# Kernel tuning notes

Hardware: AMD Instinct MI355X
Metric: run time of the kernel (lower is better)

The kernel has to match this reference:

```python
import jax, jax.numpy as jnp
import numpy as np

D_STATE = 16
D_CONV = 4
TOKEN = 8
GROUPS = 4
EPS = 1e-5


def _gn(x, w, b):
    # GroupNorm(GROUPS) over [B,C,H,W]
    B, C, H, W = x.shape
    xr = x.reshape(B, GROUPS, C // GROUPS, H * W)
    mu = xr.mean((2, 3), keepdims=True)
    var = xr.var((2, 3), keepdims=True)
    xn = ((xr - mu) * jax.lax.rsqrt(var + EPS)).reshape(B, C, H, W)
    return xn * w[None, :, None, None] + b[None, :, None, None]


def _mamba(x, in_w, conv_w, conv_b, xp_w, dt_w, dt_b, A_log, Dp, out_w, dt_rank):
    # mamba_ssm Mamba forward: x [B, L, d_model]
    Bn, L, _ = x.shape
    d_inner = conv_w.shape[0]
    xz = jnp.einsum('bld,ed->ble', x, in_w)          # [B,L,2*d_inner]
    xc, z = jnp.split(xz, 2, axis=-1)
    # causal depthwise conv1d (pad left d_conv-1)
    xt = jnp.pad(jnp.transpose(xc, (0, 2, 1)), ((0, 0), (0, 0), (D_CONV - 1, 0)))
    xt = jax.lax.conv_general_dilated(xt, conv_w[:, None, :], (1,), 'VALID',
                                      dimension_numbers=('NCH', 'OIH', 'NCH'),
                                      feature_group_count=d_inner)
    xc = jax.nn.silu(jnp.transpose(xt, (0, 2, 1)) + conv_b)
    dbl = jnp.einsum('ble,fe->blf', xc, xp_w)        # [B,L,dt_rank+2*d_state]
    dt = dbl[..., :dt_rank]
    Bm = dbl[..., dt_rank:dt_rank + D_STATE]
    Cm = dbl[..., dt_rank + D_STATE:]
    delta = jax.nn.softplus(jnp.einsum('blr,er->ble', dt, dt_w) + dt_b)
    A = -jnp.exp(A_log)                              # [d_inner, d_state]

    def step(h, inp):
        u_t, d_t, b_t, c_t = inp                     # [B,d_inner],[B,d_inner],[B,d_state],[B,d_state]
        dA = jnp.exp(d_t[..., None] * A)
        h = h * dA + (d_t * u_t)[..., None] * b_t[:, None, :]
        return h, jnp.sum(h * c_t[:, None, :], axis=-1)

    xs = (jnp.transpose(xc, (1, 0, 2)), jnp.transpose(delta, (1, 0, 2)),
          jnp.transpose(Bm, (1, 0, 2)), jnp.transpose(Cm, (1, 0, 2)))
    h0 = jnp.zeros((Bn, d_inner, D_STATE), x.dtype)
    _, ys = jax.lax.scan(step, h0, xs)
    y = (jnp.transpose(ys, (1, 0, 2)) + xc * Dp) * jax.nn.silu(z)
    return jnp.einsum('ble,de->bld', y, out_w)


def _mamba_params(key, d_model, dt_rank):
    d_inner = 2 * d_model
    ks = jax.random.split(key, 5)
    p = {}
    p['in_w'] = jax.random.normal(ks[0], (2 * d_inner, d_model)) / np.sqrt(d_model).astype(np.float32)
    p['conv_w'] = jax.random.normal(ks[1], (d_inner, D_CONV)) * 0.3
    p['conv_b'] = jnp.zeros((d_inner,))
    p['xp_w'] = jax.random.normal(ks[2], (dt_rank + 2 * D_STATE, d_inner)) / np.sqrt(d_inner).astype(np.float32)
    p['dt_w'] = jax.random.normal(ks[3], (d_inner, dt_rank)) / np.sqrt(dt_rank).astype(np.float32)
    p['dt_b'] = jnp.full((d_inner,), float(np.log(np.expm1(0.01))))
    p['A_log'] = jnp.log(jnp.broadcast_to(jnp.arange(1, D_STATE + 1, dtype=jnp.float32), (d_inner, D_STATE)))
    p['D'] = jnp.ones((d_inner,))
    p['out_w'] = jax.random.normal(ks[4], (d_model, d_inner)) / np.sqrt(d_inner).astype(np.float32)
    return p


def setup_inputs() -> dict:
    key = jax.random.key(0)
    k1, k2, k3 = jax.random.split(key, 3)
    B, C, H, W = 2, 64, 128, 128
    inp = {'x': jax.random.normal(k1, (B, C, H, W), dtype=jnp.float32)}
    spa = _mamba_params(k2, C, 4)
    spe = _mamba_params(k3, C // TOKEN, 1)
    for n, p in (('spa', spa), ('spe', spe)):
        for k, v in p.items():
            inp[f'{n}_{k}'] = v
    inp['spa_gn_w'] = jnp.ones((C,)); inp['spa_gn_b'] = jnp.zeros((C,))
    inp['spe_gn_w'] = jnp.ones((C,)); inp['spe_gn_b'] = jnp.zeros((C,))
    inp['fuse_w'] = jnp.full((2,), 0.5)
    return inp


def reference(x, spa_in_w, spa_conv_w, spa_conv_b, spa_xp_w, spa_dt_w, spa_dt_b,
              spa_A_log, spa_D, spa_out_w, spe_in_w, spe_conv_w, spe_conv_b,
              spe_xp_w, spe_dt_w, spe_dt_b, spe_A_log, spe_D, spe_out_w,
              spa_gn_w, spa_gn_b, spe_gn_w, spe_gn_b, fuse_w):
    B, C, H, W = x.shape
    # SpaMamba: scan over flattened spatial sequence
    xs = jnp.transpose(x, (0, 2, 3, 1)).reshape(B, H * W, C)
    ys = _mamba(xs, spa_in_w, spa_conv_w, spa_conv_b, spa_xp_w, spa_dt_w, spa_dt_b,
                spa_A_log, spa_D, spa_out_w, 4)
    spa = jnp.transpose(ys.reshape(B, H, W, C), (0, 3, 1, 2))
    spa = jax.nn.silu(_gn(spa, spa_gn_w, spa_gn_b)) + x
    # SpeMamba: scan over channel tokens per pixel (C == TOKEN * gc, no padding)
    gc = C // TOKEN
    xe = jnp.transpose(x, (0, 2, 3, 1)).reshape(B * H * W, TOKEN, gc)
    ye = _mamba(xe, spe_in_w, spe_conv_w, spe_conv_b, spe_xp_w, spe_dt_w, spe_dt_b,
                spe_A_log, spe_D, spe_out_w, 1)
    spe = jnp.transpose(ye.reshape(B, H, W, C), (0, 3, 1, 2))
    spe = jax.nn.silu(_gn(spe, spe_gn_w, spe_gn_b)) + x
    w = jax.nn.softmax(fuse_w)
    return spa * w[0] + spe * w[1] + x
```

## Files before the change

### kernel.cpp

```cpp
#include <hip/hip_runtime.h>
#include <math.h>


#define NB 2
#define NC 64
#define HW_ 16384
#define SCH 256
#define SLC 64

__device__ __forceinline__ float sigmoidf_(float v) { return 1.f / (1.f + __expf(-v)); }
__device__ __forceinline__ float siluf_(float v)    { return v * sigmoidf_(v); }
__device__ __forceinline__ float softplusf_(float v) {
    return v > 0.f ? v + log1pf(__expf(-v)) : log1pf(__expf(v));
}

#define K1_XS_OFF 8576
#define K1_XS_STR 68
#define K1_XCL_STR 132

__global__ __launch_bounds__(256) void k1_spatial_pre(
    const float* __restrict__ x, const float* __restrict__ in_w,
    const float* __restrict__ conv_w, const float* __restrict__ conv_b,
    const float* __restrict__ xp_w, const float* __restrict__ dt_w,
    const float* __restrict__ dt_b,
    float* __restrict__ xc_g, float* __restrict__ sz_g,
    float* __restrict__ delta_g, float* __restrict__ Bm_g, float* __restrict__ Cm_g)
{
    __shared__ float smem[13132];
    __shared__ float dtl[256];
    const int tid = threadIdx.x;
    const int b   = blockIdx.x >> 8;
    const int l0  = (blockIdx.x & 255) << 6;

    for (int i = tid; i < 67 * 64; i += 256) {
        int c = i / 67;
        int tok = i - c * 67;
        int l = l0 + tok - 3;
        float v = (l >= 0) ? x[((size_t)b * NC + c) * HW_ + l] : 0.f;
        smem[K1_XS_OFF + tok * K1_XS_STR + c] = v;
    }
    __syncthreads();

    {
        const int e = tid & 127;
        const int half = tid >> 7;
        float w[64];
        #pragma unroll
        for (int q = 0; q < 16; ++q) {
            float4 wv = *(const float4*)(in_w + e * 64 + q * 4);
            w[q*4] = wv.x; w[q*4+1] = wv.y; w[q*4+2] = wv.z; w[q*4+3] = wv.w;
        }
        int t0 = half ? 34 : 0, t1 = half ? 67 : 34;
        for (int tok = t0; tok < t1; ++tok) {
            const float4* xr = (const float4*)(smem + K1_XS_OFF + tok * K1_XS_STR);
            float acc = 0.f;
            #pragma unroll
            for (int q = 0; q < 16; ++q) {
                float4 xv = xr[q];
                acc += w[q*4]*xv.x + w[q*4+1]*xv.y + w[q*4+2]*xv.z + w[q*4+3]*xv.w;
            }
            smem[tok * 128 + e] = acc;
        }
        #pragma unroll
        for (int q = 0; q < 16; ++q) {
            float4 wv = *(const float4*)(in_w + (128 + e) * 64 + q * 4);
            w[q*4] = wv.x; w[q*4+1] = wv.y; w[q*4+2] = wv.z; w[q*4+3] = wv.w;
        }
        int z0 = half * 32;
        for (int tok = z0; tok < z0 + 32; ++tok) {
            const float4* xr = (const float4*)(smem + K1_XS_OFF + (tok + 3) * K1_XS_STR);
            float acc = 0.f;
            #pragma unroll
            for (int q = 0; q < 16; ++q) {
                float4 xv = xr[q];
                acc += w[q*4]*xv.x + w[q*4+1]*xv.y + w[q*4+2]*xv.z + w[q*4+3]*xv.w;
            }
            sz_g[((size_t)(b * HW_ + l0 + tok)) * 128 + e] = siluf_(acc);
        }
    }
    __syncthreads();

    {
        const int e = tid & 127;
        float cw0 = conv_w[e*4], cw1 = conv_w[e*4+1], cw2 = conv_w[e*4+2], cw3 = conv_w[e*4+3];
        float cb = conv_b[e];
        float r[32];
        #pragma unroll
        for (int k = 0; k < 32; ++k) {
            int tok = (tid + k * 256) >> 7;
            float v = cb + cw0 * smem[(tok+0)*128 + e] + cw1 * smem[(tok+1)*128 + e]
                         + cw2 * smem[(tok+2)*128 + e] + cw3 * smem[(tok+3)*128 + e];
            v = siluf_(v);
            r[k] = v;
            xc_g[((size_t)(b * HW_ + l0 + tok)) * 128 + e] = v;
        }
        __syncthreads();
        #pragma unroll
        for (int k = 0; k < 32; ++k) {
            int tok = (tid + k * 256) >> 7;
            smem[tok * K1_XCL_STR + e] = r[k];
        }
    }
    __syncthreads();

    for (int i = tid; i < 64 * 32; i += 256) {
        int tok = i >> 5;
        int f = i & 31;
        const float4* xr = (const float4*)(smem + tok * K1_XCL_STR);
        const float4* wr = (const float4*)(xp_w + (4 + f) * 128);
        float acc = 0.f;
        #pragma unroll
        for (int q = 0; q < 32; ++q) {
            float4 a = xr[q], w4 = wr[q];
            acc += a.x*w4.x + a.y*w4.y + a.z*w4.z + a.w*w4.w;
        }
        size_t row = (size_t)(b * HW_ + l0 + tok);
        if (f < 16) Bm_g[row * 16 + f] = acc;
        else        Cm_g[row * 16 + (f - 16)] = acc;
    }
    {
        int tok = tid >> 2;
        int rr = tid & 3;
        const float4* xr = (const float4*)(smem + tok * K1_XCL_STR);
        const float4* wr = (const float4*)(xp_w + rr * 128);
        float acc = 0.f;
        #pragma unroll
        for (int q = 0; q < 32; ++q) {
            float4 a = xr[q], w4 = wr[q];
            acc += a.x*w4.x + a.y*w4.y + a.z*w4.z + a.w*w4.w;
        }
        dtl[tid] = acc;
    }
    __syncthreads();
    {
        const int e = tid & 127;
        float w0 = dt_w[e*4], w1 = dt_w[e*4+1], w2 = dt_w[e*4+2], w3 = dt_w[e*4+3];
        float bb = dt_b[e];
        #pragma unroll
        for (int k = 0; k < 32; ++k) {
            int tok = (tid + k * 256) >> 7;
            float4 dv = *(const float4*)(dtl + tok * 4);
            float v = bb + w0*dv.x + w1*dv.y + w2*dv.z + w3*dv.w;
            delta_g[((size_t)(b * HW_ + l0 + tok)) * 128 + e] = softplusf_(v);
        }
    }
}

__global__ __launch_bounds__(256) void k2_scan1(
    const float* __restrict__ delta_g, const float* __restrict__ xc_g,
    const float* __restrict__ Bm_g, const float* __restrict__ A_log,
    float* __restrict__ cumA_g, float* __restrict__ hsum_g)
{
    const int tid = threadIdx.x;
    const int b = blockIdx.x >> 8;
    const int ch = blockIdx.x & 255;
    const int e = tid >> 1;
    const int n0 = (tid & 1) * 8;
    float A[8];
    #pragma unroll
    for (int j = 0; j < 8; ++j) A[j] = -__expf(A_log[e * 16 + n0 + j]);
    float h[8], cA[8];
    #pragma unroll
    for (int j = 0; j < 8; ++j) { h[j] = 0.f; cA[j] = 1.f; }
    const size_t rowbase = (size_t)b * HW_ + ch * SLC;
    for (int t = 0; t < SLC; ++t) {
        size_t row = rowbase + t;
        float d = delta_g[row * 128 + e];
        float u = xc_g[row * 128 + e];
        float4 b0 = *(const float4*)(Bm_g + row * 16 + n0);
        float4 b1 = *(const float4*)(Bm_g + row * 16 + n0 + 4);
        float Bv[8]; *(float4*)(Bv) = b0; *(float4*)(Bv + 4) = b1;
        float du = d * u;
        #pragma unroll
        for (int j = 0; j < 8; ++j) {
            float dA = __expf(d * A[j]);
            h[j] = h[j] * dA + du * Bv[j];
            cA[j] *= dA;
        }
    }
    size_t so = ((size_t)(b * SCH + ch)) * 2048 + tid * 8;
    #pragma unroll
    for (int j = 0; j < 8; ++j) { cumA_g[so + j] = cA[j]; hsum_g[so + j] = h[j]; }
}

__global__ __launch_bounds__(256) void k3_combine(
    const float* __restrict__ cumA_g, const float* __restrict__ hsum_g,
    float* __restrict__ Hin_g)
{
    int gid = blockIdx.x * 256 + threadIdx.x;
    int b = gid >> 11;
    int en = gid & 2047;
    float st = 0.f;
    size_t o = (size_t)b * SCH * 2048 + en;
    for (int cb = 0; cb < SCH; cb += 16) {
        float a[16], hs[16];
        #pragma unroll
        for (int k = 0; k < 16; ++k) {
            a[k]  = cumA_g[o + (size_t)k * 2048];
            hs[k] = hsum_g[o + (size_t)k * 2048];
        }
        #pragma unroll
        for (int k = 0; k < 16; ++k) {
            Hin_g[o + (size_t)k * 2048] = st;
            st = st * a[k] + hs[k];
        }
        o += (size_t)16 * 2048;
    }
}

__global__ __launch_bounds__(256) void k4_scan2(
    const float* __restrict__ delta_g, const float* __restrict__ xc_g,
    const float* __restrict__ sz_g, const float* __restrict__ Bm_g,
    const float* __restrict__ Cm_g, const float* __restrict__ A_log,
    const float* __restrict__ Dp, const float* __restrict__ Hin_g,
    const float* __restrict__ out_w,
    float* __restrict__ spa_raw, float* __restrict__ part_spa)
{
    __shared__ float ytile[SLC * 128];
    __shared__ float otile[64 * 65];
    __shared__ float wred[32];
    const int tid = threadIdx.x;
    const int b = blockIdx.x >> 8;
    const int ch = blockIdx.x & 255;
    const int e = tid >> 1;
    const int nh = tid & 1;
    const int n0 = nh * 8;
    float A[8];
    #pragma unroll
    for (int j = 0; j < 8; ++j) A[j] = -__expf(A_log[e * 16 + n0 + j]);
    float Dv = Dp[e];
    float h[8];
    size_t so = ((size_t)(b * SCH + ch)) * 2048 + tid * 8;
    #pragma unroll
    for (int j = 0; j < 8; ++j) h[j] = Hin_g[so + j];
    const size_t rowbase = (size_t)b * HW_ + ch * SLC;
    for (int t = 0; t < SLC; ++t) {
        size_t row = rowbase + t;
        float d = delta_g[row * 128 + e];
        float u = xc_g[row * 128 + e];
        float4 b0 = *(const float4*)(Bm_g + row * 16 + n0);
        float4 b1 = *(const float4*)(Bm_g + row * 16 + n0 + 4);
        float4 c0 = *(const float4*)(Cm_g + row * 16 + n0);
        float4 c1 = *(const float4*)(Cm_g + row * 16 + n0 + 4);
        float Bv[8]; *(float4*)(Bv) = b0; *(float4*)(Bv + 4) = b1;
        float Cv[8]; *(float4*)(Cv) = c0; *(float4*)(Cv + 4) = c1;
        float du = d * u;
        float y = 0.f;
        #pragma unroll
        for (int j = 0; j < 8; ++j) {
            float dA = __expf(d * A[j]);
            h[j] = h[j] * dA + du * Bv[j];
            y += h[j] * Cv[j];
        }
        y += __shfl_xor(y, 1, 64);
        if (nh == 0) {
            float szv = sz_g[row * 128 + e];
            ytile[t * 128 + e] = (y + u * Dv) * szv;
        }
    }
    __syncthreads();
    for (int i = tid; i < 64 * SLC; i += 256) {
        int c = i & 63, t = i >> 6;
        const float4* wr = (const float4*)(out_w + c * 128);
        const float4* yr = (const float4*)(ytile + t * 128);
        float acc = 0.f;
        #pragma unroll
        for (int q = 0; q < 32; ++q) {
            float4 w4 = wr[q], yv4 = yr[q];
            acc += w4.x*yv4.x + w4.y*yv4.y + w4.z*yv4.z + w4.w*yv4.w;
        }
        otile[c * 65 + t] = acc;
    }
    __syncthreads();
    for (int i = tid; i < 64 * SLC; i += 256) {
        int c = i >> 6, t = i & 63;
        spa_raw[((size_t)b * NC + c) * HW_ + ch * SLC + t] = otile[c * 65 + t];
    }
    float s[4], s2[4];
    #pragma unroll
    for (int g = 0; g < 4; ++g) {
        float a = 0.f, a2 = 0.f;
        for (int i = tid; i < 1024; i += 256) {
            int c = 16 * g + (i >> 6), t = i & 63;
            float v = otile[c * 65 + t];
            a += v; a2 += v * v;
        }
        s[g] = a; s2[g] = a2;
    }
    #pragma unroll
    for (int g = 0; g < 4; ++g) {
        #pragma unroll
        for (int o = 1; o < 64; o <<= 1) {
            s[g]  += __shfl_xor(s[g], o, 64);
            s2[g] += __shfl_xor(s2[g], o, 64);
        }
    }
    if ((tid & 63) == 0) {
        int w = tid >> 6;
        #pragma unroll
        for (int g = 0; g < 4; ++g) { wred[w*8 + g*2] = s[g]; wred[w*8 + g*2 + 1] = s2[g]; }
    }
    __syncthreads();
    if (tid < 8)
        part_spa[blockIdx.x * 8 + tid] = wred[tid] + wred[8+tid] + wred[16+tid] + wred[24+tid];
}

__global__ __launch_bounds__(256, 2) void k5_spectral(
    const float* __restrict__ x, const float* __restrict__ in_w,
    const float* __restrict__ conv_w, const float* __restrict__ conv_b,
    const float* __restrict__ xp_w, const float* __restrict__ dt_w,
    const float* __restrict__ dt_b, const float* __restrict__ A_log,
    const float* __restrict__ Dp, const float* __restrict__ out_w,
    float* __restrict__ spe_raw, float* __restrict__ part_spe)
{
    __shared__ float xin[16 * 65];
    __shared__ float ys[16 * 136];
    __shared__ float outs[64 * 17];
    __shared__ float wred[32];
    const int tid = threadIdx.x;
    const int b = blockIdx.x >> 10;
    const int hw0 = (blockIdx.x & 1023) << 4;
    const int s = tid >> 4;
    const int l = tid & 15;
    const int base = tid & 48;

    for (int i = tid; i < 1024; i += 256) {
        int c = i >> 4, j = i & 15;
        xin[j * 65 + c] = x[((size_t)b * NC + c) * HW_ + hw0 + j];
    }

    float wdt[16];
    #pragma unroll
    for (int e = 0; e < 16; ++e) wdt[e] = xp_w[e];
    float wi0[8], wi1[8];
    #pragma unroll
    for (int c = 0; c < 8; ++c) { wi0[c] = in_w[l*8 + c]; wi1[c] = in_w[(l+16)*8 + c]; }
    float cw0 = conv_w[l*4], cw1 = conv_w[l*4+1], cw2 = conv_w[l*4+2], cw3 = conv_w[l*4+3];
    float cb = conv_b[l];
    float dtw = dt_w[l], dtb = dt_b[l];
    __syncthreads();

    float pre[8], sz[8];
    #pragma unroll
    for (int t = 0; t < 8; ++t) {
        float a0 = 0.f, a1 = 0.f;
        #pragma unroll
        for (int c = 0; c < 8; ++c) {
            float xv = xin[s * 65 + t * 8 + c];
            a0 += wi0[c] * xv; a1 += wi1[c] * xv;
        }
        pre[t] = a0; sz[t] = siluf_(a1);
    }
    float xcv[8];
    #pragma unroll
    for (int t = 0; t < 8; ++t) {
        float v = cb + cw3 * pre[t];
        if (t >= 1) v += cw2 * pre[t-1];
        if (t >= 2) v += cw1 * pre[t-2];
        if (t >= 3) v += cw0 * pre[t-3];
        xcv[t] = siluf_(v);
    }

    float wB[16], wC[16];
    #pragma unroll
    for (int e = 0; e < 16; ++e) {
        wB[e] = xp_w[(1 + l) * 16 + e];
        wC[e] = xp_w[(17 + l) * 16 + e];
    }
    float bn[8], cn[8], del[8];
    #pragma unroll
    for (int t = 0; t < 8; ++t) {
        float b_ = 0.f, c_ = 0.f, d0 = 0.f;
        #pragma unroll
        for (int e = 0; e < 16; ++e) {
            float xv = __shfl(xcv[t], base + e, 64);
            b_ += wB[e] * xv; c_ += wC[e] * xv; d0 += wdt[e] * xv;
        }
        bn[t] = b_; cn[t] = c_;
        del[t] = softplusf_(d0 * dtw + dtb);
    }

    float A[16];
    #pragma unroll
    for (int n = 0; n < 16; ++n) A[n] = -__expf(A_log[l * 16 + n]);
    float Dv = Dp[l];
    float h[16];
    #pragma unroll
    for (int n = 0; n < 16; ++n) h[n] = 0.f;
    #pragma unroll
    for (int t = 0; t < 8; ++t) {
        float d = del[t], u = xcv[t];
        float du = d * u;
        float y = 0.f;
        #pragma unroll
        for (int n = 0; n < 16; ++n) {
            float Bn = __shfl(bn[t], base + n, 64);
            float Cn = __shfl(cn[t], base + n, 64);
            float dA = __expf(d * A[n]);
            h[n] = h[n] * dA + du * Bn;
            y += h[n] * Cn;
        }
        ys[s * 136 + t * 17 + l] = (y + u * Dv) * sz[t];
    }
    __syncthreads();

    {
        int t = l >> 1;
        int db = (l & 1) * 4;
        #pragma unroll
        for (int jj = 0; jj < 4; ++jj) {
            int dd = db + jj;
            float acc = 0.f;
            #pragma unroll
            for (int e = 0; e < 16; ++e) acc += out_w[dd * 16 + e] * ys[s * 136 + t * 17 + e];
            outs[(t * 8 + dd) * 17 + s] = acc;
        }
    }
    __syncthreads();

    float sg[4], sg2[4];
    #pragma unroll
    for (int k = 0; k < 4; ++k) {
        int i = tid + k * 256;
        int c = i >> 4, j = i & 15;
        float v = outs[c * 17 + j];
        spe_raw[((size_t)b * NC + c) * HW_ + hw0 + j] = v;
        sg[k] = v; sg2[k] = v * v;
    }
    #pragma unroll
    for (int k = 0; k < 4; ++k) {
        #pragma unroll
        for (int o = 1; o < 64; o <<= 1) {
            sg[k]  += __shfl_xor(sg[k], o, 64);
            sg2[k] += __shfl_xor(sg2[k], o, 64);
        }
    }
    if ((tid & 63) == 0) {
        int w = tid >> 6;
        #pragma unroll
        for (int k = 0; k < 4; ++k) { wred[w*8 + k*2] = sg[k]; wred[w*8 + k*2 + 1] = sg2[k]; }
    }
    __syncthreads();
    if (tid < 8)
        part_spe[blockIdx.x * 8 + tid] = wred[tid] + wred[8+tid] + wred[16+tid] + wred[24+tid];
}

__global__ __launch_bounds__(256) void k5b_stats(
    const float* __restrict__ part_spa, const float* __restrict__ part_spe,
    float* __restrict__ stats)
{
    __shared__ float r1[256];
    __shared__ float fin[32];
    const int tid = threadIdx.x;
    const int combo = tid >> 4, sl = tid & 15;
    const int bb = combo >> 3, g = (combo >> 1) & 3, st = combo & 1;
    float acc = 0.f;
    for (int k = 0; k < 16; ++k)
        acc += part_spa[(bb * 256 + sl * 16 + k) * 8 + g * 2 + st];
    r1[tid] = acc;
    __syncthreads();
    if (tid < 16) { float a = 0.f; for (int k = 0; k < 16; ++k) a += r1[tid*16 + k]; fin[tid] = a; }
    __syncthreads();
    acc = 0.f;
    for (int k = 0; k < 64; ++k)
        acc += part_spe[(bb * 1024 + sl * 64 + k) * 8 + g * 2 + st];
    r1[tid] = acc;
    __syncthreads();
    if (tid < 16) { float a = 0.f; for (int k = 0; k < 16; ++k) a += r1[tid*16 + k]; fin[16 + tid] = a; }
    __syncthreads();
    if (tid < 16) {
        float S  = fin[(tid >> 3) * 16 + (tid & 7) * 2];
        float S2 = fin[(tid >> 3) * 16 + (tid & 7) * 2 + 1];
        const float N = 262144.f;
        float mu = S / N;
        float var = S2 / N - mu * mu;
        stats[tid * 2] = mu;
        stats[tid * 2 + 1] = rsqrtf(var + 1e-5f);
    }
}

__global__ __launch_bounds__(256) void k6_fuse(
    const float* __restrict__ x, const float* __restrict__ spa_raw,
    const float* __restrict__ spe_raw, const float* __restrict__ stats,
    const float* __restrict__ gwa, const float* __restrict__ gba,
    const float* __restrict__ gwe, const float* __restrict__ gbe,
    const float* __restrict__ fw, float* __restrict__ out)
{
    size_t i4 = (size_t)blockIdx.x * 256 + threadIdx.x;
    size_t base = i4 * 4;
    int b = (int)(base >> 20);
    int rem = (int)(base & 1048575);
    int c = rem >> 14;
    int g = c >> 4;
    int sidx = (b * 4 + g) * 2;
    float ma = stats[sidx],      ra = stats[sidx + 1];
    float me = stats[16 + sidx], re = stats[16 + sidx + 1];
    float wa = gwa[c], ba = gba[c], we = gwe[c], be = gbe[c];
    float f0 = fw[0], f1 = fw[1];
    float mx = fmaxf(f0, f1);
    float e0 = __expf(f0 - mx), e1 = __expf(f1 - mx);
    float inv = 1.f / (e0 + e1);
    float w0 = e0 * inv, w1 = e1 * inv;
    float4 xv = *(const float4*)(x + base);
    float4 av = *(const float4*)(spa_raw + base);
    float4 ev = *(const float4*)(spe_raw + base);
    float xr[4] = {xv.x, xv.y, xv.z, xv.w};
    float ar[4] = {av.x, av.y, av.z, av.w};
    float er[4] = {ev.x, ev.y, ev.z, ev.w};
    float orr[4];
    #pragma unroll
    for (int k = 0; k < 4; ++k) {
        float spa = siluf_((ar[k] - ma) * ra * wa + ba) + xr[k];
        float spe = siluf_((er[k] - me) * re * we + be) + xr[k];
        orr[k] = spa * w0 + spe * w1 + xr[k];
    }
    float4 ov = {orr[0], orr[1], orr[2], orr[3]};
    *(float4*)(out + base) = ov;
}

extern "C" void kernel_launch(void* const* d_in, const int* in_sizes, int n_in,
                              void* d_out, int out_size, void* d_ws, size_t ws_size,
                              hipStream_t stream)
{
    const float* x      = (const float*)d_in[0];
    const float* a_inw  = (const float*)d_in[1];
    const float* a_cw   = (const float*)d_in[2];
    const float* a_cb   = (const float*)d_in[3];
    const float* a_xp   = (const float*)d_in[4];
    const float* a_dtw  = (const float*)d_in[5];
    const float* a_dtb  = (const float*)d_in[6];
    const float* a_Alog = (const float*)d_in[7];
    const float* a_D    = (const float*)d_in[8];
    const float* a_ow   = (const float*)d_in[9];
    const float* e_inw  = (const float*)d_in[10];
    const float* e_cw   = (const float*)d_in[11];
    const float* e_cb   = (const float*)d_in[12];
    const float* e_xp   = (const float*)d_in[13];
    const float* e_dtw  = (const float*)d_in[14];
    const float* e_dtb  = (const float*)d_in[15];
    const float* e_Alog = (const float*)d_in[16];
    const float* e_D    = (const float*)d_in[17];
    const float* e_ow   = (const float*)d_in[18];
    const float* gwa    = (const float*)d_in[19];
    const float* gba    = (const float*)d_in[20];
    const float* gwe    = (const float*)d_in[21];
    const float* gbe    = (const float*)d_in[22];
    const float* fw     = (const float*)d_in[23];

    float* ws    = (float*)d_ws;
    float* xc    = ws;
    float* sz    = xc    + 4194304;
    float* delta = sz    + 4194304;
    float* Bm    = delta + 4194304;
    float* Cm    = Bm    + 524288;
    float* cumA  = Cm    + 524288;
    float* hsum  = cumA  + 1048576;
    float* Hin   = hsum  + 1048576;
    float* spa_r = Hin   + 1048576;
    float* spe_r = spa_r + 2097152;
    float* pspa  = spe_r + 2097152;
    float* pspe  = pspa  + 4096;
    float* stats = pspe  + 16384;

    k1_spatial_pre<<<512, 256, 0, stream>>>(x, a_inw, a_cw, a_cb, a_xp, a_dtw, a_dtb,
                                            xc, sz, delta, Bm, Cm);
    k2_scan1<<<512, 256, 0, stream>>>(delta, xc, Bm, a_Alog, cumA, hsum);
    k3_combine<<<16, 256, 0, stream>>>(cumA, hsum, Hin);
    k5_spectral<<<2048, 256, 0, stream>>>(x, e_inw, e_cw, e_cb, e_xp, e_dtw, e_dtb,
                                          e_Alog, e_D, e_ow, spe_r, pspe);
    k4_scan2<<<512, 256, 0, stream>>>(delta, xc, sz, Bm, Cm, a_Alog, a_D, Hin, a_ow,
                                      spa_r, pspa);
    k5b_stats<<<1, 256, 0, stream>>>(pspa, pspe, stats);
    k6_fuse<<<2048, 256, 0, stream>>>(x, spa_r, spe_r, stats, gwa, gba, gwe, gbe, fw,
                                      (float*)d_out);
}
```

Before: 438.2 us.

## Recompute delta in scan kernels, stage scan inputs in LDS, halve chunk length

The full 128-wide delta tensor is no longer materialised. k1 writes only the 4-wide dt projection, and both scan kernels recompute softplus(dt_w·dt + dt_b) per step. Each chunk's xc, B, C and dt are preloaded into shared memory with coalesced float4 loads before the serial loop. The chunk length drops from 64 to 32, doubling the scan grids, which gives more parallelism but larger cumA/hsum/Hin buffers and a longer serial combine in k3. The sz gating is moved into a coalesced vectorised pass.

```diff
diff --git a/kernel.cpp b/kernel.cpp
--- a/kernel.cpp
+++ b/kernel.cpp
@@ -5,8 +5,8 @@
 #define NB 2
 #define NC 64
 #define HW_ 16384
-#define SCH 256
-#define SLC 64
+#define SCH 512
+#define SLC 32
 
 __device__ __forceinline__ float sigmoidf_(float v) { return 1.f / (1.f + __expf(-v)); }
 __device__ __forceinline__ float siluf_(float v)    { return v * sigmoidf_(v); }
@@ -21,13 +21,11 @@
 __global__ __launch_bounds__(256) void k1_spatial_pre(
     const float* __restrict__ x, const float* __restrict__ in_w,
     const float* __restrict__ conv_w, const float* __restrict__ conv_b,
-    const float* __restrict__ xp_w, const float* __restrict__ dt_w,
-    const float* __restrict__ dt_b,
+    const float* __restrict__ xp_w,
     float* __restrict__ xc_g, float* __restrict__ sz_g,
-    float* __restrict__ delta_g, float* __restrict__ Bm_g, float* __restrict__ Cm_g)
+    float* __restrict__ dtp_g, float* __restrict__ Bm_g, float* __restrict__ Cm_g)
 {
     __shared__ float smem[13132];
-    __shared__ float dtl[256];
     const int tid = threadIdx.x;
     const int b   = blockIdx.x >> 8;
     const int l0  = (blockIdx.x & 255) << 6;
@@ -129,46 +127,48 @@
             float4 a = xr[q], w4 = wr[q];
             acc += a.x*w4.x + a.y*w4.y + a.z*w4.z + a.w*w4.w;
         }
-        dtl[tid] = acc;
-    }
-    __syncthreads();
-    {
-        const int e = tid & 127;
-        float w0 = dt_w[e*4], w1 = dt_w[e*4+1], w2 = dt_w[e*4+2], w3 = dt_w[e*4+3];
-        float bb = dt_b[e];
-        #pragma unroll
-        for (int k = 0; k < 32; ++k) {
-            int tok = (tid + k * 256) >> 7;
-            float4 dv = *(const float4*)(dtl + tok * 4);
-            float v = bb + w0*dv.x + w1*dv.y + w2*dv.z + w3*dv.w;
-            delta_g[((size_t)(b * HW_ + l0 + tok)) * 128 + e] = softplusf_(v);
-        }
+        dtp_g[(size_t)(b * HW_ + l0) * 4 + tid] = acc;
     }
 }
 
 __global__ __launch_bounds__(256) void k2_scan1(
-    const float* __restrict__ delta_g, const float* __restrict__ xc_g,
-    const float* __restrict__ Bm_g, const float* __restrict__ A_log,
+    const float* __restrict__ xc_g, const float* __restrict__ Bm_g,
+    const float* __restrict__ dtp_g, const float* __restrict__ dt_w,
+    const float* __restrict__ dt_b, const float* __restrict__ A_log,
     float* __restrict__ cumA_g, float* __restrict__ hsum_g)
 {
+    __shared__ float su[SLC * 128];
+    __shared__ float sB[SLC * 16];
+    __shared__ float sdt[SLC * 4];
     const int tid = threadIdx.x;
-    const int b = blockIdx.x >> 8;
-    const int ch = blockIdx.x & 255;
+    const int b = blockIdx.x >> 9;
+    const int ch = blockIdx.x & 511;
+    const size_t rowbase = (size_t)b * HW_ + ch * SLC;
+
+    const float4* u4 = (const float4*)(xc_g + rowbase * 128);
+    #pragma unroll
+    for (int j = 0; j < 4; ++j) ((float4*)su)[tid + j * 256] = u4[tid + j * 256];
+    if (tid < 128) ((float4*)sB)[tid] = ((const float4*)(Bm_g + rowbase * 16))[tid];
+    if (tid < 32)  ((float4*)sdt)[tid] = ((const float4*)(dtp_g + rowbase * 4))[tid];
+
     const int e = tid >> 1;
     const int n0 = (tid & 1) * 8;
     float A[8];
     #pragma unroll
     for (int j = 0; j < 8; ++j) A[j] = -__expf(A_log[e * 16 + n0 + j]);
+    float4 wdt = *(const float4*)(dt_w + e * 4);
+    float dtb = dt_b[e];
     float h[8], cA[8];
     #pragma unroll
     for (int j = 0; j < 8; ++j) { h[j] = 0.f; cA[j] = 1.f; }
-    const size_t rowbase = (size_t)b * HW_ + ch * SLC;
+    __syncthreads();
+
     for (int t = 0; t < SLC; ++t) {
-        size_t row = rowbase + t;
-        float d = delta_g[row * 128 + e];
-        float u = xc_g[row * 128 + e];
-        float4 b0 = *(const float4*)(Bm_g + row * 16 + n0);
-        float4 b1 = *(const float4*)(Bm_g + row * 16 + n0 + 4);
+        float4 dv = *(const float4*)(sdt + t * 4);
+        float d = softplusf_(wdt.x*dv.x + wdt.y*dv.y + wdt.z*dv.z + wdt.w*dv.w + dtb);
+        float u = su[t * 128 + e];
+        float4 b0 = *(const float4*)(sB + t * 16 + n0);
+        float4 b1 = *(const float4*)(sB + t * 16 + n0 + 4);
         float Bv[8]; *(float4*)(Bv) = b0; *(float4*)(Bv + 4) = b1;
         float du = d * u;
         #pragma unroll
@@ -178,9 +178,11 @@
             cA[j] *= dA;
         }
     }
-    size_t so = ((size_t)(b * SCH + ch)) * 2048 + tid * 8;
-    #pragma unroll
-    for (int j = 0; j < 8; ++j) { cumA_g[so + j] = cA[j]; hsum_g[so + j] = h[j]; }
+    size_t so = (size_t)blockIdx.x * 2048 + tid * 8;
+    *(float4*)(cumA_g + so)     = *(float4*)(cA);
+    *(float4*)(cumA_g + so + 4) = *(float4*)(cA + 4);
+    *(float4*)(hsum_g + so)     = *(float4*)(h);
+    *(float4*)(hsum_g + so + 4) = *(float4*)(h + 4);
 }
 
 __global__ __launch_bounds__(256) void k3_combine(
@@ -209,39 +211,57 @@
 }
 
 __global__ __launch_bounds__(256) void k4_scan2(
-    const float* __restrict__ delta_g, const float* __restrict__ xc_g,
-    const float* __restrict__ sz_g, const float* __restrict__ Bm_g,
-    const float* __restrict__ Cm_g, const float* __restrict__ A_log,
+    const float* __restrict__ xc_g, const float* __restrict__ sz_g,
+    const float* __restrict__ Bm_g, const float* __restrict__ Cm_g,
+    const float* __restrict__ dtp_g, const float* __restrict__ dt_w,
+    const float* __restrict__ dt_b, const float* __restrict__ A_log,
     const float* __restrict__ Dp, const float* __restrict__ Hin_g,
     const float* __restrict__ out_w,
     float* __restrict__ spa_raw, float* __restrict__ part_spa)
 {
-    __shared__ float ytile[SLC * 128];
-    __shared__ float otile[64 * 65];
+    __shared__ float lds[9344];
+    float* su  = lds;
+    float* sB  = lds + 4096;
+    float* sC  = lds + 4608;
+    float* sdt = lds + 5120;
+    float* yt  = lds + 5248;
+    float* ot  = lds;
     __shared__ float wred[32];
     const int tid = threadIdx.x;
-    const int b = blockIdx.x >> 8;
-    const int ch = blockIdx.x & 255;
+    const int b = blockIdx.x >> 9;
+    const int ch = blockIdx.x & 511;
+    const size_t rowbase = (size_t)b * HW_ + ch * SLC;
+
+    const float4* u4 = (const float4*)(xc_g + rowbase * 128);
+    #pragma unroll
+    for (int j = 0; j < 4; ++j) ((float4*)su)[tid + j * 256] = u4[tid + j * 256];
+    if (tid < 128) ((float4*)sB)[tid] = ((const float4*)(Bm_g + rowbase * 16))[tid];
+    else           ((float4*)sC)[tid - 128] = ((const float4*)(Cm_g + rowbase * 16))[tid - 128];
+    if (tid < 32)  ((float4*)sdt)[tid] = ((const float4*)(dtp_g + rowbase * 4))[tid];
+
     const int e = tid >> 1;
     const int nh = tid & 1;
     const int n0 = nh * 8;
     float A[8];
     #pragma unroll
     for (int j = 0; j < 8; ++j) A[j] = -__expf(A_log[e * 16 + n0 + j]);
+    float4 wdt = *(const float4*)(dt_w + e * 4);
+    float dtb = dt_b[e];
     float Dv = Dp[e];
     float h[8];
-    size_t so = ((size_t)(b * SCH + ch)) * 2048 + tid * 8;
-    #pragma unroll
-    for (int j = 0; j < 8; ++j) h[j] = Hin_g[so + j];
-    const size_t rowbase = (size_t)b * HW_ + ch * SLC;
+    size_t so = (size_t)blockIdx.x * 2048 + tid * 8;
+    *(float4*)(h)     = *(const float4*)(Hin_g + so);
+    *(float4*)(h + 4) = *(const float4*)(Hin_g + so + 4);
+    __syncthreads();
+
     for (int t = 0; t < SLC; ++t) {
-        size_t row = rowbase + t;
-        float d = delta_g[row * 128 + e];
-        float u = xc_g[row * 128 + e];
-        float4 b0 = *(const float4*)(Bm_g + row * 16 + n0);
-        float4 b1 = *(const float4*)(Bm_g + row * 16 + n0 + 4);
-        float4 c0 = *(const float4*)(Cm_g + row * 16 + n0);
-        float4 c1 = *(const float4*)(Cm_g + row * 16 + n0 + 4);
+        float4 dv = *(const float4*)(sdt + t * 4);
+        float d = softplusf_(wdt.x*dv.x + wdt.y*dv.y + wdt.z*dv.z + wdt.w*dv.w + dtb);
+        float u = su[t * 128 + e];
+        float4 b0 = *(const float4*)(sB + t * 16 + n0);
+        float4 b1 = *(const float4*)(sB + t * 16 + n0 + 4);
+        float4 c0 = *(const float4*)(sC + t * 16 + n0);
+        float4 c1 = *(const float4*)(sC + t * 16 + n0 + 4);
         float Bv[8]; *(float4*)(Bv) = b0; *(float4*)(Bv + 4) = b1;
         float Cv[8]; *(float4*)(Cv) = c0; *(float4*)(Cv + 4) = c1;
         float du = d * u;
@@ -253,36 +273,48 @@
             y += h[j] * Cv[j];
         }
         y += __shfl_xor(y, 1, 64);
-        if (nh == 0) {
-            float szv = sz_g[row * 128 + e];
-            ytile[t * 128 + e] = (y + u * Dv) * szv;
-        }
-    }
-    __syncthreads();
+        if (nh == 0) yt[t * 128 + e] = y + u * Dv;
+    }
+    __syncthreads();
+
+    {
+        const float4* sz4 = (const float4*)(sz_g + rowbase * 128);
+        #pragma unroll
+        for (int j = 0; j < 4; ++j) {
+            int f = tid + j * 256;
+            float4 yv = ((float4*)yt)[f];
+            float4 sv = sz4[f];
+            yv.x *= sv.x; yv.y *= sv.y; yv.z *= sv.z; yv.w *= sv.w;
+            ((float4*)yt)[f] = yv;
+        }
+    }
+    __syncthreads();
+
     for (int i = tid; i < 64 * SLC; i += 256) {
         int c = i & 63, t = i >> 6;
         const float4* wr = (const float4*)(out_w + c * 128);
-        const float4* yr = (const float4*)(ytile + t * 128);
+        const float4* yr = (const float4*)(yt + t * 128);
         float acc = 0.f;
         #pragma unroll
         for (int q = 0; q < 32; ++q) {
             float4 w4 = wr[q], yv4 = yr[q];
             acc += w4.x*yv4.x + w4.y*yv4.y + w4.z*yv4.z + w4.w*yv4.w;
         }
-        otile[c * 65 + t] = acc;
-    }
-    __syncthreads();
+        ot[c * 33 + t] = acc;
+    }
+    __syncthreads();
+
     for (int i = tid; i < 64 * SLC; i += 256) {
-        int c = i >> 6, t = i & 63;
-        spa_raw[((size_t)b * NC + c) * HW_ + ch * SLC + t] = otile[c * 65 + t];
+        int c = i >> 5, t = i & 31;
+        spa_raw[((size_t)b * NC + c) * HW_ + ch * SLC + t] = ot[c * 33 + t];
     }
     float s[4], s2[4];
     #pragma unroll
     for (int g = 0; g < 4; ++g) {
         float a = 0.f, a2 = 0.f;
-        for (int i = tid; i < 1024; i += 256) {
-            int c = 16 * g + (i >> 6), t = i & 63;
-            float v = otile[c * 65 + t];
+        for (int i = tid; i < 512; i += 256) {
+            int c = 16 * g + (i >> 5), t = i & 31;
+            float v = ot[c * 33 + t];
             a += v; a2 += v * v;
         }
         s[g] = a; s2[g] = a2;
@@ -455,8 +487,8 @@
     const int combo = tid >> 4, sl = tid & 15;
     const int bb = combo >> 3, g = (combo >> 1) & 3, st = combo & 1;
     float acc = 0.f;
-    for (int k = 0; k < 16; ++k)
-        acc += part_spa[(bb * 256 + sl * 16 + k) * 8 + g * 2 + st];
+    for (int k = 0; k < 32; ++k)
+        acc += part_spa[(bb * 512 + sl * 32 + k) * 8 + g * 2 + st];
     r1[tid] = acc;
     __syncthreads();
     if (tid < 16) { float a = 0.f; for (int k = 0; k < 16; ++k) a += r1[tid*16 + k]; fin[tid] = a; }
@@ -550,26 +582,27 @@
     float* ws    = (float*)d_ws;
     float* xc    = ws;
     float* sz    = xc    + 4194304;
-    float* delta = sz    + 4194304;
-    float* Bm    = delta + 4194304;
+    float* Bm    = sz    + 4194304;
     float* Cm    = Bm    + 524288;
-    float* cumA  = Cm    + 524288;
-    float* hsum  = cumA  + 1048576;
-    float* Hin   = hsum  + 1048576;
-    float* spa_r = Hin   + 1048576;
+    float* dtp   = Cm    + 524288;
+    float* cumA  = dtp   + 131072;
+    float* hsum  = cumA  + 2097152;
+    float* Hin   = hsum  + 2097152;
+    float* spa_r = Hin   + 2097152;
     float* spe_r = spa_r + 2097152;
     float* pspa  = spe_r + 2097152;
-    float* pspe  = pspa  + 4096;
+    float* pspe  = pspa  + 8192;
     float* stats = pspe  + 16384;
 
-    k1_spatial_pre<<<512, 256, 0, stream>>>(x, a_inw, a_cw, a_cb, a_xp, a_dtw, a_dtb,
-                                            xc, sz, delta, Bm, Cm);
-    k2_scan1<<<512, 256, 0, stream>>>(delta, xc, Bm, a_Alog, cumA, hsum);
+    k1_spatial_pre<<<512, 256, 0, stream>>>(x, a_inw, a_cw, a_cb, a_xp,
+                                            xc, sz, dtp, Bm, Cm);
+    k2_scan1<<<1024, 256, 0, stream>>>(xc, Bm, dtp, a_dtw, a_dtb, a_Alog,
+                                       cumA, hsum);
     k3_combine<<<16, 256, 0, stream>>>(cumA, hsum, Hin);
     k5_spectral<<<2048, 256, 0, stream>>>(x, e_inw, e_cw, e_cb, e_xp, e_dtw, e_dtb,
                                           e_Alog, e_D, e_ow, spe_r, pspe);
-    k4_scan2<<<512, 256, 0, stream>>>(delta, xc, sz, Bm, Cm, a_Alog, a_D, Hin, a_ow,
-                                      spa_r, pspa);
+    k4_scan2<<<1024, 256, 0, stream>>>(xc, sz, Bm, Cm, dtp, a_dtw, a_dtb, a_Alog,
+                                       a_D, Hin, a_ow, spa_r, pspa);
     k5b_stats<<<1, 256, 0, stream>>>(pspa, pspe, stats);
     k6_fuse<<<2048, 256, 0, stream>>>(x, spa_r, spe_r, stats, gwa, gba, gwe, gbe, fw,
                                       (float*)d_out);
```

Measured after the change: 413.4 us. 5.7% less time.
